# Optimization experiments

Hardware: AMD Instinct MI355X
Metric: run time of the kernel (lower is better)

Reference implementation:

```python
import jax, jax.numpy as jnp
import numpy as np

B, LQ, LK, DQ, DK, DV, H = 4, 256, 512, 256, 256, 256, 128


def setup_inputs() -> dict:
    key = jax.random.key(0)
    kq, kk, kv, kwq, kwk, kwv, kl = jax.random.split(key, 7)
    queries = jax.random.normal(kq, (B, LQ, DQ), dtype=jnp.float32)
    keys = jax.random.normal(kk, (B, LK, DK), dtype=jnp.float32)
    values = jax.random.normal(kv, (B, LK, DV), dtype=jnp.float32)
    # Lazy linear params (no bias): W_q: DQ->H, W_k: DK->H, w_v: H->1
    Wq = jax.random.normal(kwq, (DQ, H), dtype=jnp.float32) / np.sqrt(DQ)
    Wk = jax.random.normal(kwk, (DK, H), dtype=jnp.float32) / np.sqrt(DK)
    wv = jax.random.normal(kwv, (H,), dtype=jnp.float32) / np.sqrt(H)
    valid_lens = jax.random.randint(kl, (B,), 1, LK + 1)
    return {"queries": queries, "keys": keys, "values": values,
            "Wq": Wq, "Wk": Wk, "wv": wv, "valid_lens": valid_lens}


def reference(queries, keys, values, Wq, Wk, wv, valid_lens):
    q = jnp.einsum('bqd,dh->bqh', queries, Wq)          # [B,LQ,H]
    k = jnp.einsum('bkd,dh->bkh', keys, Wk)             # [B,LK,H]
    # broadcast-add -> tanh -> reduce over H (the big [B,LQ,LK,H] intermediate)
    features = jnp.tanh(q[:, :, None, :] + k[:, None, :, :])
    scores = jnp.einsum('bqkh,h->bqk', features, wv)    # [B,LQ,LK]
    # masked_softmax with per-batch valid lengths (d2l semantics: masked -> -1e6)
    mask = jnp.arange(scores.shape[-1])[None, None, :] < valid_lens[:, None, None]
    scores = jnp.where(mask, scores, jnp.float32(-1e6))
    attn = jax.nn.softmax(scores, axis=-1)              # [B,LQ,LK]
    return jnp.einsum('bqk,bkv->bqv', attn, values)     # [B,LQ,DV]
```

## Files before the change

kernel.cpp:

```cpp
#include <hip/hip_runtime.h>

#define B_   4
#define LQ_  256
#define LK_  512
#define DQK_ 256
#define DV_  256
#define H_   128

#define TANH_C 2.8853900817779268f
#define L2E    1.4426950408889634f
#define NQBLK (B_ * LQ_ / 4)
#define NKBLK (B_ * LK_ / 4)

__global__ __launch_bounds__(128) void proj_kernel(const float* __restrict__ Q,
                                                   const float* __restrict__ K,
                                                   const float* __restrict__ Wq,
                                                   const float* __restrict__ Wk,
                                                   float* __restrict__ eq,
                                                   float* __restrict__ ekT) {
    const int blk = blockIdx.x;
    const bool isq = blk < NQBLK;
    const float* in = isq ? Q  : K;
    const float* W  = isq ? Wq : Wk;
    const int r0 = (isq ? blk : blk - NQBLK) * 4;
    const int t  = threadIdx.x;

    float acc0 = 0.f, acc1 = 0.f, acc2 = 0.f, acc3 = 0.f;
    const float4* in4 = reinterpret_cast<const float4*>(in + (size_t)r0 * DQK_);
    for (int d4 = 0; d4 < DQK_ / 4; ++d4) {
        float4 r0v = in4[0 * (DQK_ / 4) + d4];
        float4 r1v = in4[1 * (DQK_ / 4) + d4];
        float4 r2v = in4[2 * (DQK_ / 4) + d4];
        float4 r3v = in4[3 * (DQK_ / 4) + d4];
#pragma unroll
        for (int e = 0; e < 4; ++e) {
            float w = W[(size_t)(4 * d4 + e) * H_ + t];
            acc0 = fmaf(reinterpret_cast<const float*>(&r0v)[e], w, acc0);
            acc1 = fmaf(reinterpret_cast<const float*>(&r1v)[e], w, acc1);
            acc2 = fmaf(reinterpret_cast<const float*>(&r2v)[e], w, acc2);
            acc3 = fmaf(reinterpret_cast<const float*>(&r3v)[e], w, acc3);
        }
    }
    float e0 = __builtin_amdgcn_exp2f(acc0 * TANH_C);
    float e1 = __builtin_amdgcn_exp2f(acc1 * TANH_C);
    float e2 = __builtin_amdgcn_exp2f(acc2 * TANH_C);
    float e3 = __builtin_amdgcn_exp2f(acc3 * TANH_C);
    if (isq) {
        eq[(size_t)(r0 + 0) * H_ + t] = e0;
        eq[(size_t)(r0 + 1) * H_ + t] = e1;
        eq[(size_t)(r0 + 2) * H_ + t] = e2;
        eq[(size_t)(r0 + 3) * H_ + t] = e3;
    } else {
        const int b  = r0 >> 9;
        const int k0 = r0 & (LK_ - 1);
        float* o = ekT + ((size_t)(b * H_ + t)) * LK_ + k0;
        *reinterpret_cast<float4*>(o) = make_float4(e0, e1, e2, e3);
    }
}

__global__ __launch_bounds__(1024) void attn_kernel(
    const float* __restrict__ eq,
    const float* __restrict__ ekT,
    const float* __restrict__ wv,
    const float* __restrict__ values,
    const int*   __restrict__ valid_lens,
    float* __restrict__ out) {
    __shared__ float eq_l[4][H_];
    __shared__ float wm2[H_];
    __shared__ float sc[LK_][4];
    __shared__ float scratch[8 * 128 * 20];
    __shared__ float red[16];
    __shared__ float inv_s[4];

    float (*partB)[128][20] = reinterpret_cast<float (*)[128][20]>(scratch);
    float (*partD)[4][DV_]  = reinterpret_cast<float (*)[4][DV_]>(scratch);

    const int blk = blockIdx.x;
    const int b   = blk >> 6;
    const int qt  = blk & 63;
    const int t   = threadIdx.x;

    if (t < 512) {
        eq_l[t >> 7][t & 127] = eq[(size_t)(b * LQ_ + qt * 4 + (t >> 7)) * H_ + (t & 127)];
    } else if (t < 640) {
        wm2[t - 512] = -2.f * wv[t - 512];
    }
    __syncthreads();

    const int valid = valid_lens[b];

    {
        const int quad = t & 127;
        const int hs   = t >> 7;
        const int k0   = 4 * quad;
        float acc[16];
#pragma unroll
        for (int i = 0; i < 16; ++i) acc[i] = 0.f;

        if (k0 < valid) {
            const float* ekb = ekT + (size_t)b * H_ * LK_ + k0;
#pragma unroll 2
            for (int hh = 0; hh < 16; ++hh) {
                const int h = 16 * hs + hh;
                float4 ek = *reinterpret_cast<const float4*>(ekb + (size_t)h * LK_);
                float w = wm2[h];
#pragma unroll
                for (int r = 0; r < 4; ++r) {
                    float qv = eq_l[r][h];
                    acc[4 * r + 0] = fmaf(w, __builtin_amdgcn_rcpf(fmaf(qv, ek.x, 1.f)), acc[4 * r + 0]);
                    acc[4 * r + 1] = fmaf(w, __builtin_amdgcn_rcpf(fmaf(qv, ek.y, 1.f)), acc[4 * r + 1]);
                    acc[4 * r + 2] = fmaf(w, __builtin_amdgcn_rcpf(fmaf(qv, ek.z, 1.f)), acc[4 * r + 2]);
                    acc[4 * r + 3] = fmaf(w, __builtin_amdgcn_rcpf(fmaf(qv, ek.w, 1.f)), acc[4 * r + 3]);
                }
            }
        }
        float* pb = &partB[hs][quad][0];
#pragma unroll
        for (int i = 0; i < 4; ++i)
            *reinterpret_cast<float4*>(pb + 4 * i) = *reinterpret_cast<float4*>(&acc[4 * i]);
    }
    __syncthreads();

#pragma unroll
    for (int j = 0; j < 2; ++j) {
        const int o    = t + 1024 * j;
        const int quad = o >> 4;
        const int idx  = o & 15;
        const int k    = 4 * quad + (idx & 3);
        float s = 0.f;
#pragma unroll
        for (int hs = 0; hs < 8; ++hs) s += partB[hs][quad][idx];
        sc[k][idx >> 2] = (k < valid) ? __builtin_amdgcn_exp2f(s * L2E) : 0.f;
    }
    __syncthreads();

    const int qi = t >> 8;
    const int kl = t & 255;
    {
        float ss = sc[kl][qi] + sc[kl + 256][qi];
#pragma unroll
        for (int off = 32; off; off >>= 1) ss += __shfl_down(ss, off, 64);
        if ((t & 63) == 0) red[t >> 6] = ss;
    }
    __syncthreads();
    if (t < 4) {
        inv_s[t] = 1.f / (red[4 * t] + red[4 * t + 1] + red[4 * t + 2] + red[4 * t + 3]);
    }
    __syncthreads();

    {
        const int w  = __builtin_amdgcn_readfirstlane(t >> 6);
        const int v  = 4 * (t & 63);
        const int kstart = 32 * w;
        const int kend   = min(kstart + 32, valid);
        const float* vb = values + (size_t)b * LK_ * DV_ + v;
        float4 a0 = make_float4(0.f, 0.f, 0.f, 0.f);
        float4 a1 = a0, a2 = a0, a3 = a0;
#pragma unroll 2
        for (int k = kstart; k < kend; ++k) {
            float4 sv = *reinterpret_cast<const float4*>(&sc[k][0]);
            float4 vv = *reinterpret_cast<const float4*>(vb + (size_t)k * DV_);
            a0.x = fmaf(sv.x, vv.x, a0.x); a0.y = fmaf(sv.x, vv.y, a0.y);
            a0.z = fmaf(sv.x, vv.z, a0.z); a0.w = fmaf(sv.x, vv.w, a0.w);
            a1.x = fmaf(sv.y, vv.x, a1.x); a1.y = fmaf(sv.y, vv.y, a1.y);
            a1.z = fmaf(sv.y, vv.z, a1.z); a1.w = fmaf(sv.y, vv.w, a1.w);
            a2.x = fmaf(sv.z, vv.x, a2.x); a2.y = fmaf(sv.z, vv.y, a2.y);
            a2.z = fmaf(sv.z, vv.z, a2.z); a2.w = fmaf(sv.z, vv.w, a2.w);
            a3.x = fmaf(sv.w, vv.x, a3.x); a3.y = fmaf(sv.w, vv.y, a3.y);
            a3.z = fmaf(sv.w, vv.z, a3.z); a3.w = fmaf(sv.w, vv.w, a3.w);
        }
        *reinterpret_cast<float4*>(&partD[w][0][v]) = a0;
        *reinterpret_cast<float4*>(&partD[w][1][v]) = a1;
        *reinterpret_cast<float4*>(&partD[w][2][v]) = a2;
        *reinterpret_cast<float4*>(&partD[w][3][v]) = a3;
    }
    __syncthreads();
    {
        const int r = t >> 8;
        const int v = t & 255;
        float s = 0.f;
#pragma unroll
        for (int w = 0; w < 16; ++w) s += partD[w][r][v];
        out[(size_t)(b * LQ_ + qt * 4 + r) * DV_ + v] = s * inv_s[r];
    }
}

extern "C" void kernel_launch(void* const* d_in, const int* in_sizes, int n_in,
                              void* d_out, int out_size, void* d_ws, size_t ws_size,
                              hipStream_t stream) {
    const float* queries    = (const float*)d_in[0];
    const float* keys       = (const float*)d_in[1];
    const float* values     = (const float*)d_in[2];
    const float* Wq         = (const float*)d_in[3];
    const float* Wk         = (const float*)d_in[4];
    const float* wv         = (const float*)d_in[5];
    const int*   valid_lens = (const int*)d_in[6];
    float* out = (float*)d_out;

    float* eq  = (float*)d_ws;
    float* ekT = eq + (size_t)B_ * LQ_ * H_;

    proj_kernel<<<NQBLK + NKBLK, 128, 0, stream>>>(queries, keys, Wq, Wk, eq, ekT);
    attn_kernel<<<B_ * LQ_ / 4, 1024, 0, stream>>>(eq, ekT, wv, values, valid_lens, out);
}
```

Baseline: 28.97 us.

## Split attention over two key halves with a separate combine kernel

Result: slower. 31.23 us (+7.8%).

```diff
diff --git a/kernel.cpp b/kernel.cpp
--- a/kernel.cpp
+++ b/kernel.cpp
@@ -11,6 +11,7 @@
 #define L2E    1.4426950408889634f
 #define NQBLK (B_ * LQ_ / 4)
 #define NKBLK (B_ * LK_ / 4)
+
 
 __global__ __launch_bounds__(128) void proj_kernel(const float* __restrict__ Q,
                                                    const float* __restrict__ K,
@@ -58,47 +59,47 @@
     }
 }
 
-__global__ __launch_bounds__(1024) void attn_kernel(
+__global__ __launch_bounds__(512) void attn_half(
     const float* __restrict__ eq,
     const float* __restrict__ ekT,
     const float* __restrict__ wv,
     const float* __restrict__ values,
     const int*   __restrict__ valid_lens,
-    float* __restrict__ out) {
+    float* __restrict__ pvpart,
+    float* __restrict__ spart) {
     __shared__ float eq_l[4][H_];
     __shared__ float wm2[H_];
-    __shared__ float sc[LK_][4];
-    __shared__ float scratch[8 * 128 * 20];
-    __shared__ float red[16];
-    __shared__ float inv_s[4];
-
-    float (*partB)[128][20] = reinterpret_cast<float (*)[128][20]>(scratch);
-    float (*partD)[4][DV_]  = reinterpret_cast<float (*)[4][DV_]>(scratch);
-
-    const int blk = blockIdx.x;
-    const int b   = blk >> 6;
-    const int qt  = blk & 63;
-    const int t   = threadIdx.x;
-
-    if (t < 512) {
-        eq_l[t >> 7][t & 127] = eq[(size_t)(b * LQ_ + qt * 4 + (t >> 7)) * H_ + (t & 127)];
-    } else if (t < 640) {
-        wm2[t - 512] = -2.f * wv[t - 512];
-    }
-    __syncthreads();
-
-    const int valid = valid_lens[b];
+    __shared__ float sc[256][4];
+    __shared__ float scratch[8 * 64 * 20];
+    __shared__ float red[8];
+
+    float (*partB)[64][20] = reinterpret_cast<float (*)[64][20]>(scratch);
+    float (*partD)[4][DV_] = reinterpret_cast<float (*)[4][DV_]>(scratch);
+
+    const int blk  = blockIdx.x;
+    const int half = blk & 1;
+    const int bq   = blk >> 1;
+    const int b    = bq >> 6;
+    const int qt   = bq & 63;
+    const int t    = threadIdx.x;
+
+    eq_l[t >> 7][t & 127] = eq[(size_t)(b * LQ_ + qt * 4 + (t >> 7)) * H_ + (t & 127)];
+    if (t < H_) wm2[t] = -2.f * wv[t];
+    __syncthreads();
+
+    const int valid  = valid_lens[b];
+    const int vlocal = min(256, max(0, valid - half * 256));
 
     {
-        const int quad = t & 127;
-        const int hs   = t >> 7;
-        const int k0   = 4 * quad;
+        const int quad = t & 63;
+        const int hs   = t >> 6;
+        const int k0g  = half * 256 + 4 * quad;
         float acc[16];
 #pragma unroll
         for (int i = 0; i < 16; ++i) acc[i] = 0.f;
 
-        if (k0 < valid) {
-            const float* ekb = ekT + (size_t)b * H_ * LK_ + k0;
+        if (k0g < valid) {
+            const float* ekb = ekT + (size_t)b * H_ * LK_ + k0g;
 #pragma unroll 2
             for (int hh = 0; hh < 16; ++hh) {
                 const int h = 16 * hs + hh;
@@ -123,41 +124,41 @@
 
 #pragma unroll
     for (int j = 0; j < 2; ++j) {
-        const int o    = t + 1024 * j;
+        const int o    = t + 512 * j;
         const int quad = o >> 4;
         const int idx  = o & 15;
-        const int k    = 4 * quad + (idx & 3);
+        const int kl   = 4 * quad + (idx & 3);
         float s = 0.f;
 #pragma unroll
         for (int hs = 0; hs < 8; ++hs) s += partB[hs][quad][idx];
-        sc[k][idx >> 2] = (k < valid) ? __builtin_amdgcn_exp2f(s * L2E) : 0.f;
-    }
-    __syncthreads();
-
-    const int qi = t >> 8;
-    const int kl = t & 255;
+        sc[kl][idx >> 2] = (kl < vlocal) ? __builtin_amdgcn_exp2f(s * L2E) : 0.f;
+    }
+    __syncthreads();
+
     {
-        float ss = sc[kl][qi] + sc[kl + 256][qi];
+        const int qi = t >> 7;
+        const int kl = t & 127;
+        float ss = sc[kl][qi] + sc[kl + 128][qi];
 #pragma unroll
         for (int off = 32; off; off >>= 1) ss += __shfl_down(ss, off, 64);
         if ((t & 63) == 0) red[t >> 6] = ss;
     }
     __syncthreads();
     if (t < 4) {
-        inv_s[t] = 1.f / (red[4 * t] + red[4 * t + 1] + red[4 * t + 2] + red[4 * t + 3]);
+        spart[half * 1024 + bq * 4 + t] = red[2 * t] + red[2 * t + 1];
     }
     __syncthreads();
 
     {
-        const int w  = __builtin_amdgcn_readfirstlane(t >> 6);
-        const int v  = 4 * (t & 63);
-        const int kstart = 32 * w;
-        const int kend   = min(kstart + 32, valid);
-        const float* vb = values + (size_t)b * LK_ * DV_ + v;
+        const int w    = __builtin_amdgcn_readfirstlane(t >> 6);
+        const int v    = 4 * (t & 63);
+        const int klo  = 32 * w;
+        const int kend = min(klo + 32, vlocal);
+        const float* vb = values + ((size_t)b * LK_ + half * 256) * DV_ + v;
         float4 a0 = make_float4(0.f, 0.f, 0.f, 0.f);
         float4 a1 = a0, a2 = a0, a3 = a0;
 #pragma unroll 2
-        for (int k = kstart; k < kend; ++k) {
+        for (int k = klo; k < kend; ++k) {
             float4 sv = *reinterpret_cast<const float4*>(&sc[k][0]);
             float4 vv = *reinterpret_cast<const float4*>(vb + (size_t)k * DV_);
             a0.x = fmaf(sv.x, vv.x, a0.x); a0.y = fmaf(sv.x, vv.y, a0.y);
@@ -175,14 +176,31 @@
         *reinterpret_cast<float4*>(&partD[w][3][v]) = a3;
     }
     __syncthreads();
-    {
-        const int r = t >> 8;
-        const int v = t & 255;
+#pragma unroll
+    for (int j = 0; j < 2; ++j) {
+        const int idx = t + 512 * j;
+        const int r   = idx >> 8;
+        const int v   = idx & 255;
         float s = 0.f;
 #pragma unroll
-        for (int w = 0; w < 16; ++w) s += partD[w][r][v];
-        out[(size_t)(b * LQ_ + qt * 4 + r) * DV_ + v] = s * inv_s[r];
-    }
+        for (int w = 0; w < 8; ++w) s += partD[w][r][v];
+        pvpart[((size_t)half * 1024 + bq * 4 + r) * DV_ + v] = s;
+    }
+}
+
+__global__ __launch_bounds__(1024) void combine_kernel(
+    const float* __restrict__ pvpart,
+    const float* __restrict__ spart,
+    float* __restrict__ out) {
+    const int bq  = blockIdx.x;
+    const int t   = threadIdx.x;
+    const int r   = t >> 8;
+    const int v   = t & 255;
+    const int row = bq * 4 + r;
+    const float p = pvpart[(size_t)row * DV_ + v] +
+                    pvpart[(size_t)(1024 + row) * DV_ + v];
+    const float s = spart[row] + spart[1024 + row];
+    out[(size_t)row * DV_ + v] = p * (1.f / s);
 }
 
 extern "C" void kernel_launch(void* const* d_in, const int* in_sizes, int n_in,
@@ -197,9 +215,13 @@
     const int*   valid_lens = (const int*)d_in[6];
     float* out = (float*)d_out;
 
-    float* eq  = (float*)d_ws;
-    float* ekT = eq + (size_t)B_ * LQ_ * H_;
-
-    proj_kernel<<<NQBLK + NKBLK, 128, 0, stream>>>(queries, keys, Wq, Wk, eq, ekT);
-    attn_kernel<<<B_ * LQ_ / 4, 1024, 0, stream>>>(eq, ekT, wv, values, valid_lens, out);
-}
+    float* eq     = (float*)d_ws;
+    float* ekT    = eq     + (size_t)B_ * LQ_ * H_;
+    float* pvpart = ekT    + (size_t)B_ * H_ * LK_;
+    float* spart  = pvpart + (size_t)2 * 1024 * DV_;
+
+    proj_kernel   <<<NQBLK + NKBLK, 128, 0, stream>>>(queries, keys, Wq, Wk, eq, ekT);
+    attn_half     <<<2 * B_ * LQ_ / 4, 512, 0, stream>>>(eq, ekT, wv, values,
+                                                         valid_lens, pvpart, spart);
+    combine_kernel<<<B_ * LQ_ / 4, 1024, 0, stream>>>(pvpart, spart, out);
+}
```
